# Kernel tuning notes

Hardware: AMD Instinct MI355X
Metric: run time of the kernel (lower is better)

Reference implementation:

```python
import jax, jax.numpy as jnp
import numpy as np

EPS = 1e-5

def _face_normals(v, vi):
    # v: [B,V,3], vi: [F,3] -> [B,F,3]
    pts = v[:, vi]                                  # [B,F,3,3]
    n = jnp.cross(pts[:, :, 1] - pts[:, :, 0], pts[:, :, 2] - pts[:, :, 0])
    norm = jnp.linalg.norm(n, axis=-1, keepdims=True)
    return n / jnp.where(norm < EPS, 1.0, norm)

def _vert_normals(v, vi):
    fn = _face_normals(v, vi)                       # [B,F,3]
    fn_rep = jnp.repeat(fn, 3, axis=1)              # [B,3F,3] (one copy per face vertex)
    vn = jnp.zeros_like(v).at[:, vi.reshape(-1)].add(fn_rep)
    norm = jnp.linalg.norm(vn, axis=-1, keepdims=True)
    return vn / jnp.where(norm < EPS, 1.0, norm)

def _values_to_uv(values, index_image, bary_image):
    # values: [B,V,C]; index_image/bary_image: [U,U,3] -> [B,C,U,U]
    mask = jnp.all(index_image != -1, axis=-1)      # [U,U]
    idx = jnp.clip(index_image, 0, values.shape[1] - 1)
    vals = values[:, idx]                           # [B,U,U,3,C]
    uv = jnp.einsum('buvkc,uvk->bcuv', vals, bary_image.astype(values.dtype))
    return uv * mask[None, None].astype(values.dtype)

def _grid_sample_bilinear(img, gx, gy):
    # img: [B,C,H,W]; gx,gy: [N] in [-1,1]; align_corners=False, zero padding
    B, C, H, W = img.shape
    ix = ((gx + 1.0) * W - 1.0) * 0.5
    iy = ((gy + 1.0) * H - 1.0) * 0.5
    x0 = jnp.floor(ix); y0 = jnp.floor(iy)
    x1 = x0 + 1.0;      y1 = y0 + 1.0
    wx1 = ix - x0; wx0 = 1.0 - wx1
    wy1 = iy - y0; wy0 = 1.0 - wy1
    def gather(xi, yi):
        valid = (xi >= 0) & (xi < W) & (yi >= 0) & (yi < H)
        xc = jnp.clip(xi, 0, W - 1).astype(jnp.int32)
        yc = jnp.clip(yi, 0, H - 1).astype(jnp.int32)
        return img[:, :, yc, xc] * valid.astype(img.dtype)  # [B,C,N]
    return (gather(x0, y0) * (wx0 * wy0) + gather(x1, y0) * (wx1 * wy0)
          + gather(x0, y1) * (wx0 * wy1) + gather(x1, y1) * (wx1 * wy1))

def _sample_uv(values_uv, uv_coords, v2uv):
    g = uv_coords * 2.0 - 1.0                       # [T,2]
    vals = _grid_sample_bilinear(values_uv, g[:, 0], g[:, 1])  # [B,C,T]
    vals = jnp.transpose(vals, (0, 2, 1))           # [B,T,C]
    return vals[:, v2uv].mean(axis=2)               # [B,V,C]

def setup_inputs() -> dict:
    key = jax.random.key(0)
    ks = jax.random.split(key, 6)
    B, V, Fc, U, T, K = 8, 100000, 200000, 1024, 110000, 2
    verts = jax.random.normal(ks[0], (B, V, 3), jnp.float32)
    vi = jax.random.randint(ks[1], (Fc, 3), 0, V, dtype=jnp.int32)
    index_image = jax.random.randint(ks[2], (U, U, 3), 0, V, dtype=jnp.int32)
    bary_image = jax.random.uniform(ks[3], (U, U, 3), jnp.float32)
    vt = jax.random.uniform(ks[4], (T, 2), jnp.float32)
    v2uv = jax.random.randint(ks[5], (V, K), 0, T, dtype=jnp.int32)
    return {"verts": verts, "bary_image": bary_image, "vt": vt,
            "vi": vi, "index_image": index_image, "v2uv": v2uv}

def reference(verts, bary_image, vt, vi, index_image, v2uv):
    vn = _vert_normals(verts, vi)                   # [B,V,3]
    uv = _values_to_uv(vn, index_image, bary_image) # [B,3,U,U]
    return _sample_uv(uv, vt, v2uv)                 # [B,V,3]
```

## Files before the change

### kernel.cpp

```cpp
#include <hip/hip_runtime.h>
#include <hip/hip_fp16.h>

#define EPS 1e-5f

constexpr int B = 8;
constexpr int V = 100000;
constexpr int F = 200000;
constexpr int U = 1024;
constexpr int T = 110000;
constexpr int CAP = 24;

constexpr int NBUK = (V + 127) / 128;
constexpr int N4   = (3 * F) / 4;
constexpr int EB   = (N4 + 255) / 256;
constexpr int TRB  = (V + 255) / 256;

constexpr int FQ   = 8;
constexpr int FNB  = (F * 8 / FQ + 255) / 256;
constexpr int TQ   = 4;
constexpr int CPB  = (T / TQ + 255) / 256;
constexpr int SQ   = 2;
constexpr int VQ   = 2;

struct alignas(8) h4 { __half2 a, b; };
__device__ inline h4 pack_h4(float x, float y, float z) {
    h4 r; r.a = __floats2half2_rn(x, y); r.b = __floats2half2_rn(z, 0.0f);
    return r;
}
__device__ inline float3 unpack_h4(h4 v) {
    float2 xy = __half22float2(v.a);
    float2 zw = __half22float2(v.b);
    return make_float3(xy.x, xy.y, zw.x);
}

struct alignas(16) Corner16 { unsigned lo, hi; __half2 w01; __half2 w2_; };
__device__ inline Corner16 pack_corner(int i0, int i1, int i2,
                                       float w0, float w1, float w2) {
    unsigned long long x = (unsigned long long)(unsigned)i0
                         | ((unsigned long long)(unsigned)i1 << 21)
                         | ((unsigned long long)(unsigned)i2 << 42);
    Corner16 c;
    c.lo = (unsigned)x;
    c.hi = (unsigned)(x >> 32);
    c.w01 = __floats2half2_rn(w0, w1);
    c.w2_ = __floats2half2_rn(w2, 0.0f);
    return c;
}

__global__ void k1_pre(const float* __restrict__ verts,
                       float4* __restrict__ vertsT,
                       const int* __restrict__ vi,
                       int* __restrict__ hist) {
    __shared__ int lh[NBUK];
    int blk = blockIdx.x;
    if (blk < TRB) {
        int v = blk * 256 + threadIdx.x;
        if (v >= V) return;
        float4 row[8];
#pragma unroll
        for (int b = 0; b < 8; ++b) {
            const float* p = verts + (size_t)b * V * 3 + (size_t)v * 3;
            row[b] = make_float4(p[0], p[1], p[2], 0.0f);
        }
        float4* dst = vertsT + (size_t)v * 8;
#pragma unroll
        for (int b = 0; b < 8; ++b) dst[b] = row[b];
    } else {
        int k = blk - TRB;
        for (int i = threadIdx.x; i < NBUK; i += 256) lh[i] = 0;
        __syncthreads();
        int m4 = k * 256 + threadIdx.x;
        if (m4 < N4) {
            int4 e = ((const int4*)vi)[m4];
            atomicAdd(&lh[e.x >> 7], 1);
            atomicAdd(&lh[e.y >> 7], 1);
            atomicAdd(&lh[e.z >> 7], 1);
            atomicAdd(&lh[e.w >> 7], 1);
        }
        __syncthreads();
        for (int b = threadIdx.x; b < NBUK; b += 256) hist[k * NBUK + b] = lh[b];
    }
}

__global__ void k2_fused(const int* __restrict__ vi,
                         const float4* __restrict__ vertsT,
                         h4* __restrict__ fn,
                         const int* __restrict__ index_image,
                         const float* __restrict__ bary_image,
                         const float* __restrict__ vt,
                         Corner16* __restrict__ corners,
                         int* __restrict__ hist,
                         int* __restrict__ tot) {
    int blk = blockIdx.x;

    if (blk < FNB) {
        int id = blk * 256 + threadIdx.x;
        if (id >= F * 8 / FQ) return;
        int b = id & 7;
        int fbase = id >> 3;

        int ia[FQ], ib[FQ], ic[FQ];
        float4 p0[FQ], p1[FQ], p2[FQ];
#pragma unroll
        for (int q = 0; q < FQ; ++q) {
            int f = fbase + q * (F / FQ);
            ia[q] = vi[f * 3 + 0];
            ib[q] = vi[f * 3 + 1];
            ic[q] = vi[f * 3 + 2];
        }
#pragma unroll
        for (int q = 0; q < FQ; ++q) {
            p0[q] = vertsT[(size_t)ia[q] * 8 + b];
            p1[q] = vertsT[(size_t)ib[q] * 8 + b];
            p2[q] = vertsT[(size_t)ic[q] * 8 + b];
        }
#pragma unroll
        for (int q = 0; q < FQ; ++q) {
            int f = fbase + q * (F / FQ);
            float e1x = p1[q].x - p0[q].x, e1y = p1[q].y - p0[q].y, e1z = p1[q].z - p0[q].z;
            float e2x = p2[q].x - p0[q].x, e2y = p2[q].y - p0[q].y, e2z = p2[q].z - p0[q].z;

            float nx = e1y * e2z - e1z * e2y;
            float ny = e1z * e2x - e1x * e2z;
            float nz = e1x * e2y - e1y * e2x;

            float norm = sqrtf(nx * nx + ny * ny + nz * nz);
            float inv = (norm < EPS) ? 1.0f : (1.0f / norm);
            fn[(size_t)f * 8 + b] = pack_h4(nx * inv, ny * inv, nz * inv);
        }
        return;
    }

    if (blk < FNB + CPB) {
        int tbase = (blk - FNB) * 256 + threadIdx.x;
        if (tbase >= T / TQ) return;
#pragma unroll
        for (int qq = 0; qq < TQ; ++qq) {
            int t = tbase + qq * (T / TQ);

            float gx = vt[t * 2 + 0];
            float gy = vt[t * 2 + 1];
            float ix = gx * (float)U - 0.5f;
            float iy = gy * (float)U - 0.5f;

            float x0f = floorf(ix);
            float y0f = floorf(iy);
            int x0 = (int)x0f;
            int y0 = (int)y0f;
            float wx1 = ix - x0f, wx0 = 1.0f - wx1;
            float wy1 = iy - y0f, wy0 = 1.0f - wy1;

#pragma unroll
            for (int c = 0; c < 4; ++c) {
                int cy = c >> 1, cx = c & 1;
                int y = y0 + cy;
                int x = x0 + cx;
                int i0 = 0, i1 = 0, i2 = 0;
                float w0 = 0.0f, w1 = 0.0f, w2 = 0.0f;
                if (x >= 0 && x < U && y >= 0 && y < U) {
                    float w = (cy ? wy1 : wy0) * (cx ? wx1 : wx0);
                    int pix = y * U + x;
                    int j0 = index_image[pix * 3 + 0];
                    int j1 = index_image[pix * 3 + 1];
                    int j2 = index_image[pix * 3 + 2];
                    float m = (j0 != -1 && j1 != -1 && j2 != -1) ? 1.0f : 0.0f;
                    float wm = w * m;
                    i0 = min(max(j0, 0), V - 1);
                    i1 = min(max(j1, 0), V - 1);
                    i2 = min(max(j2, 0), V - 1);
                    w0 = wm * bary_image[pix * 3 + 0];
                    w1 = wm * bary_image[pix * 3 + 1];
                    w2 = wm * bary_image[pix * 3 + 2];
                }
                corners[t * 4 + c] = pack_corner(i0, i1, i2, w0, w1, w2);
            }
        }
        return;
    }

    {
        __shared__ int part[256];
        int b = blk - FNB - CPB;
        int th = threadIdx.x;
        int k0 = th * 3;
        int c0 = (k0     < EB) ? hist[(k0    ) * NBUK + b] : 0;
        int c1 = (k0 + 1 < EB) ? hist[(k0 + 1) * NBUK + b] : 0;
        int c2 = (k0 + 2 < EB) ? hist[(k0 + 2) * NBUK + b] : 0;
        int local = c0 + c1 + c2;
        part[th] = local;
        __syncthreads();
        for (int off = 1; off < 256; off <<= 1) {
            int x = (th >= off) ? part[th - off] : 0;
            __syncthreads();
            part[th] += x;
            __syncthreads();
        }
        int excl = part[th] - local;
        if (th == 255) tot[b] = part[255];
        if (k0     < EB) hist[(k0    ) * NBUK + b] = excl;
        if (k0 + 1 < EB) hist[(k0 + 1) * NBUK + b] = excl + c0;
        if (k0 + 2 < EB) hist[(k0 + 2) * NBUK + b] = excl + c0 + c1;
    }
}

__device__ inline void scan_base(const int* __restrict__ tot,
                                 int* pre, int* part) {
    constexpr int CH = (NBUK + 255) / 256;
    int th = threadIdx.x;
    int loc[CH];
    int local = 0;
#pragma unroll
    for (int j = 0; j < CH; ++j) {
        int idx = th * CH + j;
        int c = (idx < NBUK) ? tot[idx] : 0;
        loc[j] = local;
        local += c;
    }
    part[th] = local;
    __syncthreads();
    for (int off = 1; off < 256; off <<= 1) {
        int x = (th >= off) ? part[th - off] : 0;
        __syncthreads();
        part[th] += x;
        __syncthreads();
    }
    int excl = part[th] - local;
#pragma unroll
    for (int j = 0; j < CH; ++j) {
        int idx = th * CH + j;
        if (idx < NBUK) pre[idx] = excl + loc[j];
    }
    if (th == 255) pre[NBUK] = part[255];
    __syncthreads();
}

__global__ void k4_scatter(const int* __restrict__ vi,
                           const int* __restrict__ off,
                           const int* __restrict__ tot,
                           int* __restrict__ pairs) {
    __shared__ int lh[NBUK];
    __shared__ int pre[NBUK + 1];
    __shared__ int part[256];
    scan_base(tot, pre, part);

    int k = blockIdx.x;
    for (int i = threadIdx.x; i < NBUK; i += 256) lh[i] = 0;
    __syncthreads();
    int m4 = k * 256 + threadIdx.x;
    if (m4 >= N4) return;
    int4 e = ((const int4*)vi)[m4];
    int be = m4 * 4;
    int vv[4] = {e.x, e.y, e.z, e.w};
#pragma unroll
    for (int j = 0; j < 4; ++j) {
        int v = vv[j];
        int b = v >> 7;
        int r = atomicAdd(&lh[b], 1);
        int pos = pre[b] + off[k * NBUK + b] + r;
        pairs[pos] = ((v & 127) << 18) | ((be + j) / 3);
    }
}

__global__ __launch_bounds__(256) void k5_gather(
        const int* __restrict__ pairs,
        const int* __restrict__ tot,
        const h4* __restrict__ fn,
        h4* __restrict__ vn) {
    __shared__ int cnt[128];
    __shared__ int rows[128 * CAP];
    __shared__ int pre[NBUK + 1];
    __shared__ int part[256];
    scan_base(tot, pre, part);

    int tid = threadIdx.x;
    if (tid < 128) cnt[tid] = 0;
    __syncthreads();

    int b = blockIdx.x;
    int start = pre[b], end = pre[b + 1];
    for (int i = start + tid; i < end; i += 256) {
        int pk = pairs[i];
        int vl = pk >> 18;
        int f = pk & 0x3FFFF;
        int pos = atomicAdd(&cnt[vl], 1);
        if (pos < CAP) rows[vl * CAP + pos] = f;
    }
    __syncthreads();

    int v0 = b << 7;
    for (int id = tid; id < 128 * 8; id += 256) {
        int vl = id >> 3, b8 = id & 7;
        int v = v0 + vl;
        if (v >= V) continue;
        int deg = min(cnt[vl], CAP);
        float ax = 0.0f, ay = 0.0f, az = 0.0f;
        int j = 0;
        for (; j + 1 < deg; j += 2) {
            h4 r0 = fn[(size_t)rows[vl * CAP + j] * 8 + b8];
            h4 r1 = fn[(size_t)rows[vl * CAP + j + 1] * 8 + b8];
            float3 n0 = unpack_h4(r0);
            float3 n1 = unpack_h4(r1);
            ax += n0.x + n1.x; ay += n0.y + n1.y; az += n0.z + n1.z;
        }
        if (j < deg) {
            float3 n = unpack_h4(fn[(size_t)rows[vl * CAP + j] * 8 + b8]);
            ax += n.x; ay += n.y; az += n.z;
        }
        float nn = sqrtf(ax * ax + ay * ay + az * az);
        float inv = (nn < EPS) ? 1.0f : (1.0f / nn);
        vn[(size_t)v * 8 + b8] = pack_h4(ax * inv, ay * inv, az * inv);
    }
}

__global__ void sample_points(const h4* __restrict__ vn,
                              const Corner16* __restrict__ corners,
                              h4* __restrict__ vals) {
    int id = blockIdx.x * blockDim.x + threadIdx.x;
    if (id >= (T / SQ) * 8) return;
    int b = id & 7;
    int tb = id >> 3;

#pragma unroll
    for (int s = 0; s < SQ; ++s) {
        int t = tb + s * (T / SQ);
        float ax = 0.0f, ay = 0.0f, az = 0.0f;
        Corner16 cr[4];
#pragma unroll
        for (int c = 0; c < 4; ++c) cr[c] = corners[t * 4 + c];
        h4 q[12];
#pragma unroll
        for (int c = 0; c < 4; ++c) {
            unsigned long long x = (unsigned long long)cr[c].lo
                                 | ((unsigned long long)cr[c].hi << 32);
            int i0 = (int)(x & 0x1FFFFF);
            int i1 = (int)((x >> 21) & 0x1FFFFF);
            int i2 = (int)(x >> 42);
            q[c * 3 + 0] = vn[(size_t)i0 * 8 + b];
            q[c * 3 + 1] = vn[(size_t)i1 * 8 + b];
            q[c * 3 + 2] = vn[(size_t)i2 * 8 + b];
        }
#pragma unroll
        for (int c = 0; c < 4; ++c) {
            float2 w01 = __half22float2(cr[c].w01);
            float w2 = __low2float(cr[c].w2_);
            float3 q0 = unpack_h4(q[c * 3 + 0]);
            float3 q1 = unpack_h4(q[c * 3 + 1]);
            float3 q2 = unpack_h4(q[c * 3 + 2]);
            ax += w01.x * q0.x + w01.y * q1.x + w2 * q2.x;
            ay += w01.x * q0.y + w01.y * q1.y + w2 * q2.y;
            az += w01.x * q0.z + w01.y * q1.z + w2 * q2.z;
        }
        vals[(size_t)t * 8 + b] = pack_h4(ax, ay, az);
    }
}

__global__ void gather_out(const h4* __restrict__ vals,
                           const int* __restrict__ v2uv,
                           float* __restrict__ out) {
    int id = blockIdx.x * blockDim.x + threadIdx.x;
    if (id >= (V / VQ) * 8) return;
    int b = id & 7;
    int vb = id >> 3;

    int t0[VQ], t1[VQ];
    h4 xa[VQ], ya[VQ];
#pragma unroll
    for (int s = 0; s < VQ; ++s) {
        int v = vb + s * (V / VQ);
        t0[s] = v2uv[v * 2 + 0];
        t1[s] = v2uv[v * 2 + 1];
    }
#pragma unroll
    for (int s = 0; s < VQ; ++s) {
        xa[s] = vals[(size_t)t0[s] * 8 + b];
        ya[s] = vals[(size_t)t1[s] * 8 + b];
    }
#pragma unroll
    for (int s = 0; s < VQ; ++s) {
        int v = vb + s * (V / VQ);
        float3 x = unpack_h4(xa[s]);
        float3 y = unpack_h4(ya[s]);
        float* o = out + (size_t)b * V * 3 + (size_t)v * 3;
        o[0] = 0.5f * (x.x + y.x);
        o[1] = 0.5f * (x.y + y.y);
        o[2] = 0.5f * (x.z + y.z);
    }
}

extern "C" void kernel_launch(void* const* d_in, const int* in_sizes, int n_in,
                              void* d_out, int out_size, void* d_ws, size_t ws_size,
                              hipStream_t stream) {
    const float* verts   = (const float*)d_in[0];
    const float* bary    = (const float*)d_in[1];
    const float* vt      = (const float*)d_in[2];
    const int*   vi      = (const int*)d_in[3];
    const int*   idx_img = (const int*)d_in[4];
    const int*   v2uv    = (const int*)d_in[5];
    float* out = (float*)d_out;

    float4*   vertsT  = (float4*)d_ws;
    h4*       vn      = (h4*)d_ws;
    h4*       fn      = (h4*)(vertsT + (size_t)V * 8);
    h4*       vals    = fn;
    Corner16* corners = (Corner16*)((char*)fn + (size_t)F * 8 * sizeof(h4));
    int*      hist    = (int*)(corners + (size_t)T * 4);
    int*      tot     = hist + (size_t)EB * NBUK;
    int*      pairs   = tot + NBUK;

    const int BLK = 256;
    k1_pre<<<TRB + EB, BLK, 0, stream>>>(verts, vertsT, vi, hist);
    k2_fused<<<FNB + CPB + NBUK, BLK, 0, stream>>>(
        vi, vertsT, fn, idx_img, bary, vt, corners, hist, tot);
    k4_scatter<<<EB, BLK, 0, stream>>>(vi, hist, tot, pairs);
    k5_gather<<<NBUK, BLK, 0, stream>>>(pairs, tot, fn, vn);
    sample_points<<<((T / SQ) * 8 + BLK - 1) / BLK, BLK, 0, stream>>>(
        vn, corners, vals);
    gather_out<<<((V / VQ) * 8 + BLK - 1) / BLK, BLK, 0, stream>>>(
        vals, v2uv, out);
}
```

Before: 174.2 us.

## Replace per-block histogram scan with global atomics and restructure kernel fusion

```diff
diff --git a/kernel.cpp b/kernel.cpp
--- a/kernel.cpp
+++ b/kernel.cpp
@@ -48,24 +48,36 @@
 }
 
 __global__ void k1_pre(const float* __restrict__ verts,
-                       float4* __restrict__ vertsT,
+                       float* __restrict__ vertsT,
                        const int* __restrict__ vi,
-                       int* __restrict__ hist) {
+                       int* __restrict__ tot,
+                       const int* __restrict__ index_image,
+                       const float* __restrict__ bary_image,
+                       const float* __restrict__ vt,
+                       Corner16* __restrict__ corners) {
     __shared__ int lh[NBUK];
     int blk = blockIdx.x;
+
     if (blk < TRB) {
         int v = blk * 256 + threadIdx.x;
         if (v >= V) return;
-        float4 row[8];
+        float buf[24];
 #pragma unroll
         for (int b = 0; b < 8; ++b) {
             const float* p = verts + (size_t)b * V * 3 + (size_t)v * 3;
-            row[b] = make_float4(p[0], p[1], p[2], 0.0f);
-        }
-        float4* dst = vertsT + (size_t)v * 8;
-#pragma unroll
-        for (int b = 0; b < 8; ++b) dst[b] = row[b];
-    } else {
+            buf[b * 3 + 0] = p[0];
+            buf[b * 3 + 1] = p[1];
+            buf[b * 3 + 2] = p[2];
+        }
+        float4* dst = (float4*)(vertsT + (size_t)v * 24);
+#pragma unroll
+        for (int i = 0; i < 6; ++i)
+            dst[i] = make_float4(buf[4 * i], buf[4 * i + 1],
+                                 buf[4 * i + 2], buf[4 * i + 3]);
+        return;
+    }
+
+    if (blk < TRB + EB) {
         int k = blk - TRB;
         for (int i = threadIdx.x; i < NBUK; i += 256) lh[i] = 0;
         __syncthreads();
@@ -78,128 +90,53 @@
             atomicAdd(&lh[e.w >> 7], 1);
         }
         __syncthreads();
-        for (int b = threadIdx.x; b < NBUK; b += 256) hist[k * NBUK + b] = lh[b];
-    }
-}
-
-__global__ void k2_fused(const int* __restrict__ vi,
-                         const float4* __restrict__ vertsT,
-                         h4* __restrict__ fn,
-                         const int* __restrict__ index_image,
-                         const float* __restrict__ bary_image,
-                         const float* __restrict__ vt,
-                         Corner16* __restrict__ corners,
-                         int* __restrict__ hist,
-                         int* __restrict__ tot) {
-    int blk = blockIdx.x;
-
-    if (blk < FNB) {
-        int id = blk * 256 + threadIdx.x;
-        if (id >= F * 8 / FQ) return;
-        int b = id & 7;
-        int fbase = id >> 3;
-
-        int ia[FQ], ib[FQ], ic[FQ];
-        float4 p0[FQ], p1[FQ], p2[FQ];
-#pragma unroll
-        for (int q = 0; q < FQ; ++q) {
-            int f = fbase + q * (F / FQ);
-            ia[q] = vi[f * 3 + 0];
-            ib[q] = vi[f * 3 + 1];
-            ic[q] = vi[f * 3 + 2];
-        }
-#pragma unroll
-        for (int q = 0; q < FQ; ++q) {
-            p0[q] = vertsT[(size_t)ia[q] * 8 + b];
-            p1[q] = vertsT[(size_t)ib[q] * 8 + b];
-            p2[q] = vertsT[(size_t)ic[q] * 8 + b];
-        }
-#pragma unroll
-        for (int q = 0; q < FQ; ++q) {
-            int f = fbase + q * (F / FQ);
-            float e1x = p1[q].x - p0[q].x, e1y = p1[q].y - p0[q].y, e1z = p1[q].z - p0[q].z;
-            float e2x = p2[q].x - p0[q].x, e2y = p2[q].y - p0[q].y, e2z = p2[q].z - p0[q].z;
-
-            float nx = e1y * e2z - e1z * e2y;
-            float ny = e1z * e2x - e1x * e2z;
-            float nz = e1x * e2y - e1y * e2x;
-
-            float norm = sqrtf(nx * nx + ny * ny + nz * nz);
-            float inv = (norm < EPS) ? 1.0f : (1.0f / norm);
-            fn[(size_t)f * 8 + b] = pack_h4(nx * inv, ny * inv, nz * inv);
-        }
+        for (int b = threadIdx.x; b < NBUK; b += 256)
+            if (lh[b]) atomicAdd(&tot[b], lh[b]);
         return;
     }
 
-    if (blk < FNB + CPB) {
-        int tbase = (blk - FNB) * 256 + threadIdx.x;
-        if (tbase >= T / TQ) return;
-#pragma unroll
-        for (int qq = 0; qq < TQ; ++qq) {
-            int t = tbase + qq * (T / TQ);
-
-            float gx = vt[t * 2 + 0];
-            float gy = vt[t * 2 + 1];
-            float ix = gx * (float)U - 0.5f;
-            float iy = gy * (float)U - 0.5f;
-
-            float x0f = floorf(ix);
-            float y0f = floorf(iy);
-            int x0 = (int)x0f;
-            int y0 = (int)y0f;
-            float wx1 = ix - x0f, wx0 = 1.0f - wx1;
-            float wy1 = iy - y0f, wy0 = 1.0f - wy1;
-
-#pragma unroll
-            for (int c = 0; c < 4; ++c) {
-                int cy = c >> 1, cx = c & 1;
-                int y = y0 + cy;
-                int x = x0 + cx;
-                int i0 = 0, i1 = 0, i2 = 0;
-                float w0 = 0.0f, w1 = 0.0f, w2 = 0.0f;
-                if (x >= 0 && x < U && y >= 0 && y < U) {
-                    float w = (cy ? wy1 : wy0) * (cx ? wx1 : wx0);
-                    int pix = y * U + x;
-                    int j0 = index_image[pix * 3 + 0];
-                    int j1 = index_image[pix * 3 + 1];
-                    int j2 = index_image[pix * 3 + 2];
-                    float m = (j0 != -1 && j1 != -1 && j2 != -1) ? 1.0f : 0.0f;
-                    float wm = w * m;
-                    i0 = min(max(j0, 0), V - 1);
-                    i1 = min(max(j1, 0), V - 1);
-                    i2 = min(max(j2, 0), V - 1);
-                    w0 = wm * bary_image[pix * 3 + 0];
-                    w1 = wm * bary_image[pix * 3 + 1];
-                    w2 = wm * bary_image[pix * 3 + 2];
-                }
-                corners[t * 4 + c] = pack_corner(i0, i1, i2, w0, w1, w2);
+    int tbase = (blk - TRB - EB) * 256 + threadIdx.x;
+    if (tbase >= T / TQ) return;
+#pragma unroll
+    for (int qq = 0; qq < TQ; ++qq) {
+        int t = tbase + qq * (T / TQ);
+
+        float gx = vt[t * 2 + 0];
+        float gy = vt[t * 2 + 1];
+        float ix = gx * (float)U - 0.5f;
+        float iy = gy * (float)U - 0.5f;
+
+        float x0f = floorf(ix);
+        float y0f = floorf(iy);
+        int x0 = (int)x0f;
+        int y0 = (int)y0f;
+        float wx1 = ix - x0f, wx0 = 1.0f - wx1;
+        float wy1 = iy - y0f, wy0 = 1.0f - wy1;
+
+#pragma unroll
+        for (int c = 0; c < 4; ++c) {
+            int cy = c >> 1, cx = c & 1;
+            int y = y0 + cy;
+            int x = x0 + cx;
+            int i0 = 0, i1 = 0, i2 = 0;
+            float w0 = 0.0f, w1 = 0.0f, w2 = 0.0f;
+            if (x >= 0 && x < U && y >= 0 && y < U) {
+                float w = (cy ? wy1 : wy0) * (cx ? wx1 : wx0);
+                int pix = y * U + x;
+                int j0 = index_image[pix * 3 + 0];
+                int j1 = index_image[pix * 3 + 1];
+                int j2 = index_image[pix * 3 + 2];
+                float m = (j0 != -1 && j1 != -1 && j2 != -1) ? 1.0f : 0.0f;
+                float wm = w * m;
+                i0 = min(max(j0, 0), V - 1);
+                i1 = min(max(j1, 0), V - 1);
+                i2 = min(max(j2, 0), V - 1);
+                w0 = wm * bary_image[pix * 3 + 0];
+                w1 = wm * bary_image[pix * 3 + 1];
+                w2 = wm * bary_image[pix * 3 + 2];
             }
-        }
-        return;
-    }
-
-    {
-        __shared__ int part[256];
-        int b = blk - FNB - CPB;
-        int th = threadIdx.x;
-        int k0 = th * 3;
-        int c0 = (k0     < EB) ? hist[(k0    ) * NBUK + b] : 0;
-        int c1 = (k0 + 1 < EB) ? hist[(k0 + 1) * NBUK + b] : 0;
-        int c2 = (k0 + 2 < EB) ? hist[(k0 + 2) * NBUK + b] : 0;
-        int local = c0 + c1 + c2;
-        part[th] = local;
-        __syncthreads();
-        for (int off = 1; off < 256; off <<= 1) {
-            int x = (th >= off) ? part[th - off] : 0;
-            __syncthreads();
-            part[th] += x;
-            __syncthreads();
-        }
-        int excl = part[th] - local;
-        if (th == 255) tot[b] = part[255];
-        if (k0     < EB) hist[(k0    ) * NBUK + b] = excl;
-        if (k0 + 1 < EB) hist[(k0 + 1) * NBUK + b] = excl + c0;
-        if (k0 + 2 < EB) hist[(k0 + 2) * NBUK + b] = excl + c0 + c1;
+            corners[t * 4 + c] = pack_corner(i0, i1, i2, w0, w1, w2);
+        }
     }
 }
 
@@ -234,30 +171,87 @@
     __syncthreads();
 }
 
-__global__ void k4_scatter(const int* __restrict__ vi,
-                           const int* __restrict__ off,
-                           const int* __restrict__ tot,
-                           int* __restrict__ pairs) {
-    __shared__ int lh[NBUK];
+__global__ __launch_bounds__(256, 2) void k2_fused(
+        const int* __restrict__ vi,
+        const float* __restrict__ vertsT,
+        h4* __restrict__ fn,
+        const int* __restrict__ tot,
+        int* __restrict__ cursor,
+        int* __restrict__ pairs) {
+    int blk = blockIdx.x;
+
+    if (blk < FNB) {
+        int id = blk * 256 + threadIdx.x;
+        if (id >= F * 8 / FQ) return;
+        int b = id & 7;
+        int fbase = id >> 3;
+        const float3* vT = (const float3*)vertsT;
+
+        int ia[FQ], ib[FQ], ic[FQ];
+        float3 p0[FQ], p1[FQ], p2[FQ];
+#pragma unroll
+        for (int q = 0; q < FQ; ++q) {
+            int f = fbase + q * (F / FQ);
+            ia[q] = vi[f * 3 + 0];
+            ib[q] = vi[f * 3 + 1];
+            ic[q] = vi[f * 3 + 2];
+        }
+#pragma unroll
+        for (int q = 0; q < FQ; ++q) {
+            p0[q] = vT[(size_t)ia[q] * 8 + b];
+            p1[q] = vT[(size_t)ib[q] * 8 + b];
+            p2[q] = vT[(size_t)ic[q] * 8 + b];
+        }
+#pragma unroll
+        for (int q = 0; q < FQ; ++q) {
+            int f = fbase + q * (F / FQ);
+            float e1x = p1[q].x - p0[q].x, e1y = p1[q].y - p0[q].y, e1z = p1[q].z - p0[q].z;
+            float e2x = p2[q].x - p0[q].x, e2y = p2[q].y - p0[q].y, e2z = p2[q].z - p0[q].z;
+
+            float nx = e1y * e2z - e1z * e2y;
+            float ny = e1z * e2x - e1x * e2z;
+            float nz = e1x * e2y - e1y * e2x;
+
+            float norm = sqrtf(nx * nx + ny * ny + nz * nz);
+            float inv = (norm < EPS) ? 1.0f : (1.0f / norm);
+            fn[(size_t)f * 8 + b] = pack_h4(nx * inv, ny * inv, nz * inv);
+        }
+        return;
+    }
+
     __shared__ int pre[NBUK + 1];
     __shared__ int part[256];
+    __shared__ int lh[NBUK];
+    __shared__ int base[NBUK];
     scan_base(tot, pre, part);
-
-    int k = blockIdx.x;
     for (int i = threadIdx.x; i < NBUK; i += 256) lh[i] = 0;
     __syncthreads();
+
+    int k = blk - FNB;
     int m4 = k * 256 + threadIdx.x;
-    if (m4 >= N4) return;
-    int4 e = ((const int4*)vi)[m4];
-    int be = m4 * 4;
-    int vv[4] = {e.x, e.y, e.z, e.w};
-#pragma unroll
-    for (int j = 0; j < 4; ++j) {
-        int v = vv[j];
-        int b = v >> 7;
-        int r = atomicAdd(&lh[b], 1);
-        int pos = pre[b] + off[k * NBUK + b] + r;
-        pairs[pos] = ((v & 127) << 18) | ((be + j) / 3);
+    bool act = (m4 < N4);
+    int vv[4], rr[4], bbk[4], fc[4];
+    if (act) {
+        int4 e = ((const int4*)vi)[m4];
+        vv[0] = e.x; vv[1] = e.y; vv[2] = e.z; vv[3] = e.w;
+        int be = m4 * 4;
+#pragma unroll
+        for (int j = 0; j < 4; ++j) {
+            bbk[j] = vv[j] >> 7;
+            rr[j] = atomicAdd(&lh[bbk[j]], 1);
+            fc[j] = (be + j) / 3;
+        }
+    }
+    __syncthreads();
+    for (int i = threadIdx.x; i < NBUK; i += 256)
+        base[i] = lh[i] ? atomicAdd(&cursor[i], lh[i]) : 0;
+    __syncthreads();
+    if (act) {
+#pragma unroll
+        for (int j = 0; j < 4; ++j) {
+            int pos = pre[bbk[j]] + base[bbk[j]] + rr[j];
+            pairs[pos] = ((vv[j] & 127) << 18) | fc[j];
+        }
     }
 }
 
@@ -398,20 +392,20 @@
     const int*   v2uv    = (const int*)d_in[5];
     float* out = (float*)d_out;
 
-    float4*   vertsT  = (float4*)d_ws;
+    float*    vertsT  = (float*)d_ws;
     h4*       vn      = (h4*)d_ws;
-    h4*       fn      = (h4*)(vertsT + (size_t)V * 8);
+    h4*       fn      = (h4*)((char*)d_ws + (size_t)V * 8 * 12);
     h4*       vals    = fn;
     Corner16* corners = (Corner16*)((char*)fn + (size_t)F * 8 * sizeof(h4));
-    int*      hist    = (int*)(corners + (size_t)T * 4);
-    int*      tot     = hist + (size_t)EB * NBUK;
-    int*      pairs   = tot + NBUK;
+    int*      tot     = (int*)(corners + (size_t)T * 4);
+    int*      cursor  = tot + NBUK;
+    int*      pairs   = cursor + NBUK;
 
     const int BLK = 256;
-    k1_pre<<<TRB + EB, BLK, 0, stream>>>(verts, vertsT, vi, hist);
-    k2_fused<<<FNB + CPB + NBUK, BLK, 0, stream>>>(
-        vi, vertsT, fn, idx_img, bary, vt, corners, hist, tot);
-    k4_scatter<<<EB, BLK, 0, stream>>>(vi, hist, tot, pairs);
+    hipMemsetAsync(tot, 0, 2 * NBUK * sizeof(int), stream);
+    k1_pre<<<TRB + EB + CPB, BLK, 0, stream>>>(
+        verts, vertsT, vi, tot, idx_img, bary, vt, corners);
+    k2_fused<<<FNB + EB, BLK, 0, stream>>>(vi, vertsT, fn, tot, cursor, pairs);
     k5_gather<<<NBUK, BLK, 0, stream>>>(pairs, tot, fn, vn);
     sample_points<<<((T / SQ) * 8 + BLK - 1) / BLK, BLK, 0, stream>>>(
         vn, corners, vals);
```

After: 186.2 us. 1.07x slower.
